# Optimization experiments

Measured on AMD Instinct MI355X. Metric: run time of the kernel, lower is better.

## Reference

```python
import jax, jax.numpy as jnp
import numpy as np
from jax import lax

GAMMA = 0.01
BIG = 1e8  # stand-in for +inf on DP borders (keeps grads finite/zero)


def _pairwise_sq_dists(x, y):
    # x: [N,1] (target), y: [N,1] (pred) -> D[i,j] = (x_i - y_j)^2
    xn = jnp.sum(x * x, axis=1)  # [N]
    yn = jnp.sum(y * y, axis=1)  # [N]
    d = xn[:, None] + yn[None, :] - 2.0 * (x @ y.T)
    return jnp.maximum(d, 0.0)


def _soft_dtw(D, gamma):
    # Soft-DTW DP via wavefront scan over the 2N-1 anti-diagonals.
    # R[i,j] = D[i,j] + softmin_gamma(R[i-1,j-1], R[i-1,j], R[i,j-1]),
    # with virtual R[-1,-1] = 0 and +inf borders.
    N = D.shape[0]
    ii = jnp.arange(N)

    def shift(r):  # r[i] -> r[i-1], BIG at i=0
        return jnp.concatenate([jnp.full((1,), BIG, r.dtype), r[:-1]])

    def step(carry, k):
        r1, r2 = carry  # diagonals k-1 and k-2, indexed by row i
        jj = k - ii
        valid = (jj >= 0) & (jj < N)
        d = D[ii, jnp.clip(jj, 0, N - 1)]
        a = shift(r2)                                   # R[i-1, j-1]
        a = jnp.where((k == 0) & (ii == 0), 0.0, a)     # virtual origin
        b = shift(r1)                                   # R[i-1, j]
        c = jnp.where(jj >= 1, r1, BIG)                 # R[i, j-1]
        vals = jnp.stack([a, b, c])                     # [3, N]
        m = jnp.min(vals, axis=0)
        softmin = m - gamma * jnp.log(jnp.sum(jnp.exp(-(vals - m) / gamma), axis=0))
        r_new = jnp.where(valid, d + softmin, BIG)
        return (r_new, r1), None

    init = jnp.full((N,), BIG, D.dtype)
    (r_last, _), _ = lax.scan(step, (init, init), jnp.arange(2 * N - 1))
    return r_last[N - 1]  # R[N-1, N-1], batch size 1 -> mean == value


def setup_inputs() -> dict:
    key = jax.random.key(0)
    k1, k2 = jax.random.split(key)
    pred = jax.random.normal(k1, (4096, 1), dtype=jnp.float32)
    target = jax.random.normal(k2, (4096, 1), dtype=jnp.float32)
    return {"pred": pred, "target": target}


def reference(pred, target):
    # DILATELoss.forward returns loss_shape (the soft-DTW value);
    # the temporal path term is computed in the original but discarded.
    D = _pairwise_sq_dists(target.reshape(-1, 1), pred.reshape(-1, 1))
    return _soft_dtw(D, GAMMA)
```

## Files before the change

kernel.cpp:

```cpp
#include <hip/hip_runtime.h>

#define NN    4096
#define BIGF  1e8f
#define SQK2f 12.0112245225638540f
#define BIGK  1.4426950408889634e10f
#define IK2f  0.00693147180559945309f
#define NBLK  32
#define NCI   132
#define SKEW  72
#define OUTS  4167
#define SENTU 0xFFFFFFFFu

__global__ __launch_bounds__(1024) void dilate_sdtw(const float* __restrict__ pred,
                                                    const float* __restrict__ target,
                                                    float* __restrict__ out) {
    __shared__ float t_s[NN];
    __shared__ float p_s[NN];
    __shared__ float bufA[NN];
    __shared__ float bufB[NN];
    __shared__ float bufC[NN];
    const int tid = threadIdx.x;
    for (int i = tid; i < NN; i += 1024) {
        t_s[i] = target[i]; p_s[i] = pred[i];
        bufA[i] = BIGF; bufB[i] = BIGF; bufC[i] = BIGF;
    }
    __syncthreads();
    float* r2 = bufA; float* r1 = bufB; float* rn = bufC;
    for (int k = 0; k < 2 * NN - 1; ++k) {
        int ilo = k - (NN - 1); if (ilo < 0) ilo = 0;
        int ihi = (k < NN - 1) ? k : (NN - 1);
        for (int i = ilo + tid; i <= ihi; i += 1024) {
            const int j = k - i;
            float diff = t_s[i] - p_s[j];
            float d = diff * diff;
            float a = (i >= 1 && j >= 1) ? r2[i - 1] : ((k == 0) ? 0.0f : BIGF);
            float b = (i >= 1) ? r1[i - 1] : BIGF;
            float c = (j >= 1) ? r1[i] : BIGF;
            float m = fminf(a, fminf(b, c));
            float s = __expf((m - a) * 100.0f) + __expf((m - b) * 100.0f) + __expf((m - c) * 100.0f);
            rn[i] = d + m - 0.01f * __logf(s);
        }
        __syncthreads();
        float* tmp = r2; r2 = r1; r1 = rn; rn = tmp;
    }
    if (tid == 0) out[0] = r1[NN - 1];
}


__device__ __forceinline__ float softmin3s(float a, float b, float c) {
    float m = fminf(a, fminf(b, c));
    float e = __builtin_amdgcn_exp2f(m - a)
            + __builtin_amdgcn_exp2f(m - b)
            + __builtin_amdgcn_exp2f(m - c);
    return m - __builtin_amdgcn_logf(e);
}

__device__ __forceinline__ void bput(float* p, float v) {
    __hip_atomic_store((unsigned int*)p, __float_as_uint(v),
                       __ATOMIC_RELAXED, __HIP_MEMORY_SCOPE_AGENT);
}
__device__ __forceinline__ unsigned int bgetu(const float* p) {
    return __hip_atomic_load((const unsigned int*)p,
                             __ATOMIC_RELAXED, __HIP_MEMORY_SCOPE_AGENT);
}

__device__ __forceinline__ void uissue(const float* src, float* dst) {
#pragma unroll
    for (int q = 0; q < 32; ++q) dst[q] = __uint_as_float(bgetu(src + q));
}
__device__ __forceinline__ bool uvalid(const float* dst) {
    bool ok = true;
#pragma unroll
    for (int q = 0; q < 32; ++q) ok &= (__float_as_uint(dst[q]) != SENTU);
    return ok;
}
__device__ __forceinline__ void upoll(const float* src, float* dst) {
    for (;;) {
        uissue(src, dst);
        if (uvalid(dst)) return;
        __builtin_amdgcn_s_sleep(1);
    }
}

__device__ __forceinline__ void pload(const float* p_s, int base, float* dst) {
#pragma unroll
    for (int q = 0; q < 32; ++q) {
        int idx = base + q;
        idx = idx < 0 ? 0 : (idx > NN - 1 ? NN - 1 : idx);
        dst[q] = p_s[idx];
    }
}

template<bool TOP, bool BOT, bool EDGE>
__device__ __forceinline__ void chunk32(
    int cs, int lane, int off, bool l0, float t0, float t1,
    float& v0, float& v1, float& u2, float& sh1, float& sh2, float& sh3, float upl,
    float4& acc, const float* upc, const float* pc,
    float* __restrict__ bnd_my, float* __restrict__ outp)
{
#pragma unroll
    for (int u = 0; u < 32; ++u) {
        const int s = cs + u;
        const int j = s - off;
        float u1 = __int_as_float(__builtin_amdgcn_update_dpp(
            __float_as_int(sh3), __float_as_int(v1), 0x111, 0xF, 0xF, false));
        float shN = __shfl_up(v1, 1);
        float a, b;
        if (TOP) {
            a = l0 ? ((s == 0) ? 0.0f : BIGK) : u2;
            b = l0 ? BIGK : u1;
        } else {
            float upj  = upc[u];
            float upjm = (u == 0) ? upl : upc[u - 1];
            a = l0 ? upjm : u2;
            b = l0 ? upj  : u1;
        }
        float pj = pc[u];
        float d0 = t0 - pj;
        float val0 = fmaf(d0, d0, softmin3s(a, b, v0));
        float d1 = t1 - pj;
        float val1 = fmaf(d1, d1, softmin3s(v0, val0, v1));
        if (EDGE) {
            bool vj = (unsigned)j < (unsigned)NN;
            val0 = vj ? val0 : BIGK;
            val1 = vj ? val1 : BIGK;
        }
        if (!BOT) {
            switch (u & 3) {
                case 0: acc.x = val1; break;
                case 1: acc.y = val1; break;
                case 2: acc.z = val1; break;
                case 3: acc.w = val1; break;
            }
            if ((u & 3) == 3) {
                int base = j - 3;
                if (lane == 63 && (!EDGE || (unsigned)base <= (unsigned)(NN - 4))) {
                    bput(bnd_my + base + 0, acc.x);
                    bput(bnd_my + base + 1, acc.y);
                    bput(bnd_my + base + 2, acc.z);
                    bput(bnd_my + base + 3, acc.w);
                }
            }
        } else if (EDGE) {
            if (lane == 63 && s == OUTS) outp[0] = val1 * IK2f;
        }
        v0 = val0; v1 = val1; u2 = u1;
        sh3 = sh2; sh2 = sh1; sh1 = shN;
    }
}

template<bool TOP, bool BOT>
__device__ __forceinline__ void chunk_iter(
    int ci, int lane, int off, bool l0, float t0, float t1,
    float& v0, float& v1, float& u2, float& sh1, float& sh2, float& sh3, float& upl,
    float4& acc,
    float* upC, float* upN, float* pcC, float* pcN,
    const float* p_s, const float* __restrict__ bnd_up, float* __restrict__ bnd_my,
    float* __restrict__ outp)
{
    const int cs = 32 * ci;
    if (!TOP && cs < NN) {
        if (!uvalid(upC)) upoll(bnd_up + cs, upC);
        if (cs + 32 < NN) uissue(bnd_up + cs + 32, upN);
    }
    if (ci + 1 < NCI) pload(p_s, cs + 32 - off, pcN);

    const bool edge = (ci < 4) || (ci >= 128);
    if (edge) chunk32<TOP, BOT, true >(cs, lane, off, l0, t0, t1, v0, v1, u2,
                                       sh1, sh2, sh3, upl, acc, upC, pcC, bnd_my, outp);
    else      chunk32<TOP, BOT, false>(cs, lane, off, l0, t0, t1, v0, v1, u2,
                                       sh1, sh2, sh3, upl, acc, upC, pcC, bnd_my, outp);
    if (!TOP) upl = upC[31];
}

template<bool TOP, bool BOT>
__device__ void stripe(int b, int lane, const float* __restrict__ target,
                       const float* p_s, float* bnd, float* outp)
{
    const int off = (lane & 15) + 19 * (lane >> 4);
    const float t0 = target[128 * b + 2 * lane]     * SQK2f;
    const float t1 = target[128 * b + 2 * lane + 1] * SQK2f;
    float* bnd_my = bnd + (size_t)b * NN;
    const float* bnd_up = bnd + (size_t)(b - 1) * NN;
    const bool l0 = (lane == 0);

    float v0 = BIGK, v1 = BIGK, u2 = BIGK, upl = BIGK;
    float sh1 = BIGK, sh2 = BIGK, sh3 = BIGK;
    float4 acc = {BIGK, BIGK, BIGK, BIGK};
    float upA[32], upB[32];
    float pcA[32], pcB[32];

    pload(p_s, -off, pcA);
    if (!TOP) uissue(bnd_up, upA);

    for (int cp = 0; cp < NCI / 2; ++cp) {
        chunk_iter<TOP, BOT>(2 * cp,     lane, off, l0, t0, t1, v0, v1, u2,
                             sh1, sh2, sh3, upl, acc,
                             upA, upB, pcA, pcB, p_s, bnd_up, bnd_my, outp);
        chunk_iter<TOP, BOT>(2 * cp + 1, lane, off, l0, t0, t1, v0, v1, u2,
                             sh1, sh2, sh3, upl, acc,
                             upB, upA, pcB, pcA, p_s, bnd_up, bnd_my, outp);
    }
}

__global__ __launch_bounds__(64, 1) void sdtw_pipe8(const float* __restrict__ pred,
                                                    const float* __restrict__ target,
                                                    float* __restrict__ out,
                                                    float* __restrict__ bnd)
{
    __shared__ float p_s[NN];
    const int lane = threadIdx.x;
    const int bid = blockIdx.x;
    const int b = (bid & 7) * 4 + (bid >> 3);
    for (int i = lane; i < NN; i += 64) p_s[i] = pred[i] * SQK2f;
    __syncthreads();
    if (b == 0)                stripe<true , false>(b, lane, target, p_s, bnd, out);
    else if (b == NBLK - 1)    stripe<false, true >(b, lane, target, p_s, bnd, out);
    else                       stripe<false, false>(b, lane, target, p_s, bnd, out);
}

extern "C" void kernel_launch(void* const* d_in, const int* in_sizes, int n_in,
                              void* d_out, int out_size, void* d_ws, size_t ws_size,
                              hipStream_t stream) {
    const float* pred   = (const float*)d_in[0];
    const float* target = (const float*)d_in[1];
    float* out = (float*)d_out;

    const size_t need = (size_t)NBLK * NN * sizeof(float);
    if (ws_size >= need) {
        float* bnd = (float*)d_ws;
        hipMemsetAsync(d_ws, 0xFF, need, stream);
        sdtw_pipe8<<<dim3(NBLK), dim3(64), 0, stream>>>(pred, target, out, bnd);
    } else {
        dilate_sdtw<<<dim3(1), dim3(1024), 0, stream>>>(pred, target, out);
    }
}
```

Before: 935.8 us.

## Replace skewed lane offsets with unit skew using DPP row shift and row broadcast

```diff
diff --git a/kernel.cpp b/kernel.cpp
--- a/kernel.cpp
+++ b/kernel.cpp
@@ -6,9 +6,8 @@
 #define BIGK  1.4426950408889634e10f
 #define IK2f  0.00693147180559945309f
 #define NBLK  32
-#define NCI   132
-#define SKEW  72
-#define OUTS  4167
+#define NCI   130
+#define OUTS  4158
 #define SENTU 0xFFFFFFFFu
 
 __global__ __launch_bounds__(1024) void dilate_sdtw(const float* __restrict__ pred,
@@ -55,6 +54,13 @@
     return m - __builtin_amdgcn_logf(e);
 }
 
+__device__ __forceinline__ float nbr1(float v, bool bsel) {
+    int iv = __float_as_int(v);
+    float a = __int_as_float(__builtin_amdgcn_update_dpp(iv, iv, 0x111, 0xF, 0xF, false));
+    float b = __int_as_float(__builtin_amdgcn_update_dpp(iv, iv, 0x142, 0xF, 0xF, false));
+    return bsel ? b : a;
+}
+
 __device__ __forceinline__ void bput(float* p, float v) {
     __hip_atomic_store((unsigned int*)p, __float_as_uint(v),
                        __ATOMIC_RELAXED, __HIP_MEMORY_SCOPE_AGENT);
@@ -93,18 +99,15 @@
 
 template<bool TOP, bool BOT, bool EDGE>
 __device__ __forceinline__ void chunk32(
-    int cs, int lane, int off, bool l0, float t0, float t1,
-    float& v0, float& v1, float& u2, float& sh1, float& sh2, float& sh3, float upl,
+    int cs, int lane, bool l0, bool bsel, float t0, float t1,
+    float& v0, float& v1, float& u1, float& u2, float upl,
     float4& acc, const float* upc, const float* pc,
     float* __restrict__ bnd_my, float* __restrict__ outp)
 {
 #pragma unroll
     for (int u = 0; u < 32; ++u) {
         const int s = cs + u;
-        const int j = s - off;
-        float u1 = __int_as_float(__builtin_amdgcn_update_dpp(
-            __float_as_int(sh3), __float_as_int(v1), 0x111, 0xF, 0xF, false));
-        float shN = __shfl_up(v1, 1);
+        const int j = s - lane;
         float a, b;
         if (TOP) {
             a = l0 ? ((s == 0) ? 0.0f : BIGK) : u2;
@@ -126,13 +129,13 @@
             val1 = vj ? val1 : BIGK;
         }
         if (!BOT) {
-            switch (u & 3) {
+            switch ((u + 1) & 3) {
                 case 0: acc.x = val1; break;
                 case 1: acc.y = val1; break;
                 case 2: acc.z = val1; break;
                 case 3: acc.w = val1; break;
             }
-            if ((u & 3) == 3) {
+            if ((u & 3) == 2) {
                 int base = j - 3;
                 if (lane == 63 && (!EDGE || (unsigned)base <= (unsigned)(NN - 4))) {
                     bput(bnd_my + base + 0, acc.x);
@@ -144,15 +147,16 @@
         } else if (EDGE) {
             if (lane == 63 && s == OUTS) outp[0] = val1 * IK2f;
         }
-        v0 = val0; v1 = val1; u2 = u1;
-        sh3 = sh2; sh2 = sh1; sh1 = shN;
+        v0 = val0; v1 = val1;
+        u2 = u1;
+        u1 = nbr1(val1, bsel);
     }
 }
 
 template<bool TOP, bool BOT>
 __device__ __forceinline__ void chunk_iter(
-    int ci, int lane, int off, bool l0, float t0, float t1,
-    float& v0, float& v1, float& u2, float& sh1, float& sh2, float& sh3, float& upl,
+    int ci, int lane, bool l0, bool bsel, float t0, float t1,
+    float& v0, float& v1, float& u1, float& u2, float& upl,
     float4& acc,
     float* upC, float* upN, float* pcC, float* pcN,
     const float* p_s, const float* __restrict__ bnd_up, float* __restrict__ bnd_my,
@@ -163,13 +167,13 @@
         if (!uvalid(upC)) upoll(bnd_up + cs, upC);
         if (cs + 32 < NN) uissue(bnd_up + cs + 32, upN);
     }
-    if (ci + 1 < NCI) pload(p_s, cs + 32 - off, pcN);
-
-    const bool edge = (ci < 4) || (ci >= 128);
-    if (edge) chunk32<TOP, BOT, true >(cs, lane, off, l0, t0, t1, v0, v1, u2,
-                                       sh1, sh2, sh3, upl, acc, upC, pcC, bnd_my, outp);
-    else      chunk32<TOP, BOT, false>(cs, lane, off, l0, t0, t1, v0, v1, u2,
-                                       sh1, sh2, sh3, upl, acc, upC, pcC, bnd_my, outp);
+    if (ci + 1 < NCI) pload(p_s, cs + 32 - lane, pcN);
+
+    const bool edge = (ci < 2) || (ci >= 128);
+    if (edge) chunk32<TOP, BOT, true >(cs, lane, l0, bsel, t0, t1, v0, v1, u1, u2,
+                                       upl, acc, upC, pcC, bnd_my, outp);
+    else      chunk32<TOP, BOT, false>(cs, lane, l0, bsel, t0, t1, v0, v1, u1, u2,
+                                       upl, acc, upC, pcC, bnd_my, outp);
     if (!TOP) upl = upC[31];
 }
 
@@ -177,33 +181,30 @@
 __device__ void stripe(int b, int lane, const float* __restrict__ target,
                        const float* p_s, float* bnd, float* outp)
 {
-    const int off = (lane & 15) + 19 * (lane >> 4);
     const float t0 = target[128 * b + 2 * lane]     * SQK2f;
     const float t1 = target[128 * b + 2 * lane + 1] * SQK2f;
     float* bnd_my = bnd + (size_t)b * NN;
     const float* bnd_up = bnd + (size_t)(b - 1) * NN;
     const bool l0 = (lane == 0);
-
-    float v0 = BIGK, v1 = BIGK, u2 = BIGK, upl = BIGK;
-    float sh1 = BIGK, sh2 = BIGK, sh3 = BIGK;
+    const bool bsel = (lane != 0) && ((lane & 15) == 0);
+
+    float v0 = BIGK, v1 = BIGK, u1 = BIGK, u2 = BIGK, upl = BIGK;
     float4 acc = {BIGK, BIGK, BIGK, BIGK};
     float upA[32], upB[32];
     float pcA[32], pcB[32];
 
-    pload(p_s, -off, pcA);
+    pload(p_s, -lane, pcA);
     if (!TOP) uissue(bnd_up, upA);
 
     for (int cp = 0; cp < NCI / 2; ++cp) {
-        chunk_iter<TOP, BOT>(2 * cp,     lane, off, l0, t0, t1, v0, v1, u2,
-                             sh1, sh2, sh3, upl, acc,
+        chunk_iter<TOP, BOT>(2 * cp,     lane, l0, bsel, t0, t1, v0, v1, u1, u2, upl, acc,
                              upA, upB, pcA, pcB, p_s, bnd_up, bnd_my, outp);
-        chunk_iter<TOP, BOT>(2 * cp + 1, lane, off, l0, t0, t1, v0, v1, u2,
-                             sh1, sh2, sh3, upl, acc,
+        chunk_iter<TOP, BOT>(2 * cp + 1, lane, l0, bsel, t0, t1, v0, v1, u1, u2, upl, acc,
                              upB, upA, pcB, pcA, p_s, bnd_up, bnd_my, outp);
     }
 }
 
-__global__ __launch_bounds__(64, 1) void sdtw_pipe8(const float* __restrict__ pred,
+__global__ __launch_bounds__(64, 1) void sdtw_pipe9(const float* __restrict__ pred,
                                                     const float* __restrict__ target,
                                                     float* __restrict__ out,
                                                     float* __restrict__ bnd)
@@ -230,7 +231,7 @@
     if (ws_size >= need) {
         float* bnd = (float*)d_ws;
         hipMemsetAsync(d_ws, 0xFF, need, stream);
-        sdtw_pipe8<<<dim3(NBLK), dim3(64), 0, stream>>>(pred, target, out, bnd);
+        sdtw_pipe9<<<dim3(NBLK), dim3(64), 0, stream>>>(pred, target, out, bnd);
     } else {
         dilate_sdtw<<<dim3(1), dim3(1024), 0, stream>>>(pred, target, out);
     }
```

After: 858.3 us. 1.09x faster.
